# Performance work log

Hardware: AMD Instinct MI355X
Metric: run time of the kernel (lower is better)

The kernel has to match this reference:

```python
import jax
import jax.numpy as jnp
from jax import lax
import numpy as np

NUM_LABELS = 128
PAD, BOS, EOS = 0, 1, 2
B, T = 512, 512
NEG = -10000.0


def setup_inputs() -> dict:
    key = jax.random.key(0)
    k1, k2, k3, k4 = jax.random.split(key, 4)
    features = jax.random.normal(k1, (B, T, NUM_LABELS), dtype=jnp.float32)
    tag_seqs = jax.random.randint(k2, (B, T), 0, NUM_LABELS, dtype=jnp.int32)
    # prefix-valid mask with variable lengths in [T//2, T]
    lengths = jax.random.randint(k3, (B,), T // 2, T + 1, dtype=jnp.int32)
    mask = jnp.arange(T, dtype=jnp.int32)[None, :] < lengths[:, None]
    # transitions: randn then the constrained rows/cols from CRF.__init__
    tr = jax.random.normal(k4, (NUM_LABELS, NUM_LABELS), dtype=jnp.float32)
    tr = tr.at[:, BOS].set(NEG)
    tr = tr.at[EOS, :].set(NEG)
    tr = tr.at[PAD, :].set(NEG)
    tr = tr.at[:, PAD].set(NEG)
    tr = tr.at[PAD, PAD].set(0.0)
    tr = tr.at[PAD, EOS].set(0.0)
    return {"features": features, "tag_seqs": tag_seqs, "mask": mask, "transitions": tr}


def _crf_nll(features, transitions, tag_seqs, mask):
    maskf = mask.astype(features.dtype)  # [B,T]
    # ---- gold path score (score_sentences), fully vectorized over time ----
    emis = jnp.take_along_axis(features, tag_seqs[..., None], axis=-1)[..., 0]  # [B,T]
    trans_steps = transitions[tag_seqs[:, :-1], tag_seqs[:, 1:]]               # [B,T-1]
    gold = emis[:, 0] + transitions[BOS, tag_seqs[:, 0]]
    gold = gold + jnp.sum(maskf[:, 1:] * (emis[:, 1:] + trans_steps), axis=1)
    vlen = jnp.sum(mask.astype(jnp.int32), axis=1) - 1                          # [B]
    last_lab = jnp.take_along_axis(tag_seqs, vlen[:, None], axis=1)[:, 0]
    gold = gold + transitions[last_lab, EOS]
    # ---- log-partition (forward_alg): sequential scan over time ----
    init = transitions[BOS, :][None, :] + features[:, 0]  # [B,L]

    def step(fv, xs):
        feat_t, m_t = xs  # [B,L], [B] bool
        # scores[b, prev, cur] = fv[b,prev] + trans[prev,cur] + emit[b,cur]
        scores = fv[:, :, None] + transitions[None, :, :] + feat_t[:, None, :]
        new_fv = jax.nn.logsumexp(scores, axis=1)  # [B,L]
        fv = jnp.where(m_t[:, None], new_fv, fv)
        return fv, None

    xs = (jnp.swapaxes(features[:, 1:], 0, 1), jnp.swapaxes(mask[:, 1:], 0, 1))
    fv, _ = lax.scan(step, init, xs)
    logZ = jax.nn.logsumexp(fv + transitions[:, EOS][None, :], axis=-1)  # [B]
    return -jnp.mean(gold - logZ)


def reference(features, tag_seqs, mask, transitions):
    return _crf_nll(features, transitions, tag_seqs, mask)
```

## Files before the change

kernel.cpp:

```cpp
#include <hip/hip_runtime.h>
#include <cstdint>
#include <cstddef>

#define NLAB 128
#define TT   512
#define BB   512
#define MB   16
#define PAD_ 0
#define BOS_ 1
#define EOS_ 2
#define LN2F  0.6931471805599453f
#define LOG2E 1.4426950408889634f

typedef float f32x4 __attribute__((ext_vector_type(4)));
typedef short s16x8 __attribute__((ext_vector_type(8)));

#if __has_builtin(__builtin_amdgcn_exp2f)
#define EXP2F(x) __builtin_amdgcn_exp2f(x)
#else
#define EXP2F(x) exp2f(x)
#endif

#define MFMA_(A,B,CV) __builtin_amdgcn_mfma_f32_16x16x32_bf16((A),(B),(CV),0,0,0)

__device__ __forceinline__ bool mask_is_i32(const unsigned char* m8) {
    return m8[1] == 0;
}
__device__ __forceinline__ bool mask_at(const unsigned char* m8, int idx, bool isi) {
    if (isi) return ((const int*)m8)[idx] != 0;
    return m8[idx] != 0;
}

__device__ __forceinline__ unsigned f2bf(float f) {
    union { float f; unsigned u; } v; v.f = f;
    return (v.u + 0x7FFFu + ((v.u >> 16) & 1u)) >> 16;
}
__device__ __forceinline__ unsigned cvtpk(float lo, float hi) {
    unsigned r;
    asm("v_cvt_pk_bf16_f32 %0, %1, %2" : "=v"(r) : "v"(lo), "v"(hi));
    return r;
}

__global__ __launch_bounds__(256, 1) void crf_fused(
        const float* __restrict__ feats,
        const int*   __restrict__ tags,
        const unsigned char* __restrict__ m8,
        const float* __restrict__ tr,
        float* __restrict__ gold_out,
        float* __restrict__ logZ_out) {
    const int bx  = blockIdx.x;
    const int tid = threadIdx.x;
    const bool isi = mask_is_i32(m8);

    if (bx >= BB / MB) {
        const int b    = (bx - BB / MB) * 4 + (tid >> 6);
        const int lane = tid & 63;
        const size_t fb = (size_t)b * TT * NLAB;
        float gp = 0.f; int cnt = 0;
        for (int tt = lane; tt < TT; tt += 64) {
            const int idx = b * TT + tt;
            const bool mm = mask_at(m8, idx, isi);
            cnt += mm ? 1 : 0;
            const int tg = tags[idx];
            if (tt == 0) gp += feats[fb + tg] + tr[BOS_ * NLAB + tg];
            else if (mm) gp += feats[fb + (size_t)tt * NLAB + tg]
                             + tr[tags[idx - 1] * NLAB + tg];
        }
        #pragma unroll
        for (int off = 32; off > 0; off >>= 1) {
            gp  += __shfl_xor(gp,  off, 64);
            cnt += __shfl_xor(cnt, off, 64);
        }
        if (lane == 0)
            gold_out[b] = gp + tr[tags[b * TT + cnt - 1] * NLAB + EOS_];
        return;
    }

    const int w = tid >> 6;
    const int l = tid & 63;
    const int a = l >> 4;
    const int c = l & 15;
    const int G = bx * MB + c;
    const size_t fbase = (size_t)G * TT * NLAB;

    __shared__ __align__(16) unsigned short P16[2][2048];
    __shared__ float red_s[4][MB];

    f32x4 F0a, F0b, F1a, F1b, F2a, F2b, F3a, F3b,
          F4a, F4b, F5a, F5b, F6a, F6b, F7a, F7b;
    {
        const f32x4* fp = (const f32x4*)(feats + fbase);
        const int s0 = 4 * w + a, s1 = 4 * w + 16 + a;
        F0a = fp[1 * 32 + s0]; F0b = fp[1 * 32 + s1];
        F1a = fp[2 * 32 + s0]; F1b = fp[2 * 32 + s1];
        F2a = fp[3 * 32 + s0]; F2b = fp[3 * 32 + s1];
        F3a = fp[4 * 32 + s0]; F3b = fp[4 * 32 + s1];
        F4a = fp[5 * 32 + s0]; F4b = fp[5 * 32 + s1];
        F5a = fp[6 * 32 + s0]; F5b = fp[6 * 32 + s1];
        F6a = fp[7 * 32 + s0]; F6b = fp[7 * 32 + s1];
        F7a = fp[8 * 32 + s0]; F7b = fp[8 * 32 + s1];
    }

    int cnt = 0;
    if (isi) {
        const uint4* mp = (const uint4*)((const int*)m8 + (size_t)G * TT + a * 128);
        #pragma unroll 8
        for (int i = 0; i < 32; ++i) {
            uint4 v = mp[i];
            cnt += (v.x != 0) + (v.y != 0) + (v.z != 0) + (v.w != 0);
        }
    } else {
        const uint4* mp = (const uint4*)(m8 + (size_t)G * TT + a * 128);
        #pragma unroll
        for (int i = 0; i < 8; ++i) {
            uint4 v = mp[i];
            cnt += (int)((((v.x & 0x01010101u) * 0x01010101u) >> 24)
                       + (((v.y & 0x01010101u) * 0x01010101u) >> 24)
                       + (((v.z & 0x01010101u) * 0x01010101u) >> 24)
                       + (((v.w & 0x01010101u) * 0x01010101u) >> 24));
        }
    }
    cnt += __shfl_xor(cnt, 16, 64);
    cnt += __shfl_xor(cnt, 32, 64);
    const int mylen = cnt;
    int maxlen = mylen;
    maxlen = max(maxlen, __shfl_xor(maxlen, 1, 64));
    maxlen = max(maxlen, __shfl_xor(maxlen, 2, 64));
    maxlen = max(maxlen, __shfl_xor(maxlen, 4, 64));
    maxlen = max(maxlen, __shfl_xor(maxlen, 8, 64));
    const int mx = maxlen - 1;

    s16x8 Af00, Af01, Af02, Af03, Af10, Af11, Af12, Af13;
    {
        s16x8* A0[4] = {&Af00, &Af01, &Af02, &Af03};
        s16x8* A1[4] = {&Af10, &Af11, &Af12, &Af13};
        #pragma unroll
        for (int kt = 0; kt < 4; ++kt)
            #pragma unroll
            for (int jj = 0; jj < 8; ++jj) {
                const float* tp = tr + (kt * 32 + a * 8 + jj) * NLAB + c;
                (*A0[kt])[jj] = (short)f2bf(__expf(tp[w * 16]));
                (*A1[kt])[jj] = (short)f2bf(__expf(tp[(w + 4) * 16]));
            }
    }

    f32x4 pf0, pf1;
    float C;
    {
        const float n0 = tr[BOS_ * NLAB + 3] + feats[fbase + 3];
        C = n0;
        const f32x4 tb0 = *(const f32x4*)(tr + BOS_ * NLAB + w * 16 + a * 4);
        const f32x4 ff0 = *(const f32x4*)(feats + fbase + w * 16 + a * 4);
        const f32x4 tb1 = *(const f32x4*)(tr + BOS_ * NLAB + (w + 4) * 16 + a * 4);
        const f32x4 ff1 = *(const f32x4*)(feats + fbase + (w + 4) * 16 + a * 4);
        #pragma unroll
        for (int r = 0; r < 4; ++r) {
            pf0[r] = __expf(tb0[r] + ff0[r] - n0);
            pf1[r] = __expf(tb1[r] + ff1[r] - n0);
        }
    }

    const int wb0 = ((2 * w       + (a >> 1)) * 16 + c) * 8 + (a & 1) * 4;
    const int wb1 = ((2 * (w + 4) + (a >> 1)) * 16 + c) * 8 + (a & 1) * 4;
    *(uint2*)&P16[0][wb0] = make_uint2(cvtpk(pf0[0], pf0[1]), cvtpk(pf0[2], pf0[3]));
    *(uint2*)&P16[0][wb1] = make_uint2(cvtpk(pf1[0], pf1[1]), cvtpk(pf1[2], pf1[3]));

    const int rab = a * 16 + c;
    const f32x4 zac = {0.f, 0.f, 0.f, 0.f};

#define STEP(T_, Fa, Fb) {                                                    \
    __syncthreads();                                                          \
    const int PB = (T_) & 1;                                                  \
    const s16x8* PR = (const s16x8*)P16[1 - PB];                              \
    const s16x8 b0 = PR[rab],       b1 = PR[64 + rab],                        \
                b2 = PR[128 + rab], b3 = PR[192 + rab];                       \
    const int efield = ((int)(unsigned short)b0[3] >> 7) & 255;               \
    const int e = __shfl(efield, c, 64) - 126;                                \
    f32x4 x0 = MFMA_(Af00, b0, zac); x0 = MFMA_(Af01, b1, x0);                \
    f32x4 y0 = MFMA_(Af02, b2, zac); y0 = MFMA_(Af03, b3, y0);                \
    f32x4 x1 = MFMA_(Af10, b0, zac); x1 = MFMA_(Af11, b1, x1);                \
    f32x4 y1 = MFMA_(Af12, b2, zac); y1 = MFMA_(Af13, b3, y1);                \
    const float sc = __uint_as_float((unsigned)(127 - e) << 23);    \
    const f32x4 acc0 = x0 + y0, acc1 = x1 + y1;                               \
    const bool live = (T_) < mylen;                                           \
    _Pragma("unroll")                                                         \
    for (int r = 0; r < 4; ++r) {                                             \
        const float q0 = acc0[r] * (EXP2F(Fa[r] * LOG2E) * sc);               \
        const float q1 = acc1[r] * (EXP2F(Fb[r] * LOG2E) * sc);               \
        if (live) { pf0[r] = q0; pf1[r] = q1; }                               \
    }                                                                         \
    if (live) C += (float)e * LN2F;                                           \
    *(uint2*)&P16[PB][wb0] = make_uint2(cvtpk(pf0[0], pf0[1]),                \
                                        cvtpk(pf0[2], pf0[3]));               \
    *(uint2*)&P16[PB][wb1] = make_uint2(cvtpk(pf1[0], pf1[1]),                \
                                        cvtpk(pf1[2], pf1[3]));               \
}

    #pragma unroll 1
    for (int t0 = 1; t0 < maxlen; t0 += 8) {
        const int nstep = min(8, maxlen - t0);
        STEP(t0, F0a, F0b)
        if (nstep > 1) STEP(t0 + 1, F1a, F1b)
        if (nstep > 2) STEP(t0 + 2, F2a, F2b)
        if (nstep > 3) STEP(t0 + 3, F3a, F3b)
        if (nstep > 4) STEP(t0 + 4, F4a, F4b)
        if (nstep > 5) STEP(t0 + 5, F5a, F5b)
        if (nstep > 6) STEP(t0 + 6, F6a, F6b)
        if (nstep > 7) STEP(t0 + 7, F7a, F7b)
        if (t0 + 8 < maxlen) {
            const int s0 = 4 * w + a, s1 = 4 * w + 16 + a;
            const f32x4* fp;
#define RF(i, Xa, Xb)                                                         \
            fp = (const f32x4*)(feats + fbase                                 \
                     + (size_t)min(t0 + 8 + (i), mx) * NLAB);                 \
            Xa = fp[s0]; Xb = fp[s1];
            RF(0, F0a, F0b) RF(1, F1a, F1b) RF(2, F2a, F2b) RF(3, F3a, F3b)
            RF(4, F4a, F4b) RF(5, F5a, F5b) RF(6, F6a, F6b) RF(7, F7a, F7b)
#undef RF
        }
    }
#undef STEP

    float s = 0.f;
    #pragma unroll
    for (int r = 0; r < 4; ++r) {
        s += pf0[r] * __expf(tr[(w * 16 + 4 * a + r) * NLAB + EOS_]);
        s += pf1[r] * __expf(tr[((w + 4) * 16 + 4 * a + r) * NLAB + EOS_]);
    }
    s += __shfl_xor(s, 16, 64);
    s += __shfl_xor(s, 32, 64);
    if (l < 16) red_s[w][c] = s;
    __syncthreads();
    if (tid < 16) {
        float S = red_s[0][tid] + red_s[1][tid] + red_s[2][tid] + red_s[3][tid];
        logZ_out[bx * MB + tid] = C + __logf(S);
    }
}

__global__ void crf_finalize(const float* __restrict__ gold,
                             const float* __restrict__ logZ,
                             float* __restrict__ out) {
    __shared__ float sh[4];
    const int i = threadIdx.x;
    float v = (logZ[i] - gold[i]) + (logZ[i + 256] - gold[i + 256]);
    #pragma unroll
    for (int off = 32; off > 0; off >>= 1)
        v += __shfl_xor(v, off, 64);
    if ((i & 63) == 0) sh[i >> 6] = v;
    __syncthreads();
    if (i == 0) out[0] = (sh[0] + sh[1] + sh[2] + sh[3]) * (1.0f / (float)BB);
}

extern "C" void kernel_launch(void* const* d_in, const int* in_sizes, int n_in,
                              void* d_out, int out_size, void* d_ws, size_t ws_size,
                              hipStream_t stream) {
    const float*         feats = (const float*)d_in[0];
    const int*           tags  = (const int*)d_in[1];
    const unsigned char* m8    = (const unsigned char*)d_in[2];
    const float*         tr    = (const float*)d_in[3];

    float* gold = (float*)d_ws;
    float* logZ = gold + BB;
    float* out  = (float*)d_out;

    hipLaunchKernelGGL(crf_fused, dim3(BB / MB + BB / 4), dim3(256), 0, stream,
                       feats, tags, m8, tr, gold, logZ);
    hipLaunchKernelGGL(crf_finalize, dim3(1), dim3(256), 0, stream,
                       gold, logZ, out);
}
```

Measured before the change: 411.1 us.

## Stream feature prefetch per step and precompute next-step exponentials off critical path

Replaces the batched 8-step feature reload with a rolling per-step prefetch of the feature row eight steps ahead into the register that was just consumed. The emission exponential for the next step is computed after the LDS write, moving it off the critical path between barrier and MFMA result. The MFMA chain is split into eight independent products summed afterward, and the scale exponent is read straight from LDS instead of through a shuffle. This trades more frequent global loads and extra register pressure for shorter dependent latency inside each sequential scan step.

```diff
diff --git a/kernel.cpp b/kernel.cpp
--- a/kernel.cpp
+++ b/kernel.cpp
@@ -86,11 +86,12 @@
     __shared__ __align__(16) unsigned short P16[2][2048];
     __shared__ float red_s[4][MB];
 
+    const int s0 = 4 * w + a, s1 = 4 * w + 16 + a;
+
     f32x4 F0a, F0b, F1a, F1b, F2a, F2b, F3a, F3b,
           F4a, F4b, F5a, F5b, F6a, F6b, F7a, F7b;
     {
         const f32x4* fp = (const f32x4*)(feats + fbase);
-        const int s0 = 4 * w + a, s1 = 4 * w + 16 + a;
         F0a = fp[1 * 32 + s0]; F0b = fp[1 * 32 + s1];
         F1a = fp[2 * 32 + s0]; F1b = fp[2 * 32 + s1];
         F2a = fp[3 * 32 + s0]; F2b = fp[3 * 32 + s1];
@@ -165,28 +166,41 @@
     *(uint2*)&P16[0][wb0] = make_uint2(cvtpk(pf0[0], pf0[1]), cvtpk(pf0[2], pf0[3]));
     *(uint2*)&P16[0][wb1] = make_uint2(cvtpk(pf1[0], pf1[1]), cvtpk(pf1[2], pf1[3]));
 
+    #pragma unroll
+    for (int r = 0; r < 4; ++r) {
+        F0a[r] = EXP2F(F0a[r] * LOG2E);
+        F0b[r] = EXP2F(F0b[r] * LOG2E);
+    }
+
     const int rab = a * 16 + c;
     const f32x4 zac = {0.f, 0.f, 0.f, 0.f};
 
-#define STEP(T_, Fa, Fb) {                                                    \
+#define STEP(T_, Fa, Fb, Na, Nb) {                                            \
     __syncthreads();                                                          \
+    const f32x4 efa = Fa, efb = Fb;          \
+    {   const f32x4* fp = (const f32x4*)(feats + fbase                        \
+                              + (size_t)min((T_) + 8, mx) * NLAB);            \
+        Fa = fp[s0]; Fb = fp[s1]; }                                           \
     const int PB = (T_) & 1;                                                  \
     const s16x8* PR = (const s16x8*)P16[1 - PB];                              \
     const s16x8 b0 = PR[rab],       b1 = PR[64 + rab],                        \
                 b2 = PR[128 + rab], b3 = PR[192 + rab];                       \
-    const int efield = ((int)(unsigned short)b0[3] >> 7) & 255;               \
-    const int e = __shfl(efield, c, 64) - 126;                                \
-    f32x4 x0 = MFMA_(Af00, b0, zac); x0 = MFMA_(Af01, b1, x0);                \
-    f32x4 y0 = MFMA_(Af02, b2, zac); y0 = MFMA_(Af03, b3, y0);                \
-    f32x4 x1 = MFMA_(Af10, b0, zac); x1 = MFMA_(Af11, b1, x1);                \
-    f32x4 y1 = MFMA_(Af12, b2, zac); y1 = MFMA_(Af13, b3, y1);                \
+    const int p3 = (int)P16[1 - PB][c * 8 + 3];                               \
+    f32x4 x0 = MFMA_(Af00, b0, zac); f32x4 x1 = MFMA_(Af01, b1, zac);         \
+    f32x4 x2 = MFMA_(Af02, b2, zac); f32x4 x3 = MFMA_(Af03, b3, zac);         \
+    f32x4 y0 = MFMA_(Af10, b0, zac); f32x4 y1 = MFMA_(Af11, b1, zac);         \
+    f32x4 y2 = MFMA_(Af12, b2, zac); f32x4 y3 = MFMA_(Af13, b3, zac);         \
+    const int e = ((p3 >> 7) & 255) - 126;                                    \
     const float sc = __uint_as_float((unsigned)(127 - e) << 23);    \
-    const f32x4 acc0 = x0 + y0, acc1 = x1 + y1;                               \
+    const f32x4 acc0 = (x0 + x1) + (x2 + x3);                                 \
+    const f32x4 acc1 = (y0 + y1) + (y2 + y3);                                 \
     const bool live = (T_) < mylen;                                           \
     _Pragma("unroll")                                                         \
     for (int r = 0; r < 4; ++r) {                                             \
-        const float q0 = acc0[r] * (EXP2F(Fa[r] * LOG2E) * sc);               \
-        const float q1 = acc1[r] * (EXP2F(Fb[r] * LOG2E) * sc);               \
+        const float m0 = efa[r] * sc;      \
+        const float m1 = efb[r] * sc;                                         \
+        const float q0 = acc0[r] * m0;                                        \
+        const float q1 = acc1[r] * m1;                                        \
         if (live) { pf0[r] = q0; pf1[r] = q1; }                               \
     }                                                                         \
     if (live) C += (float)e * LN2F;                                           \
@@ -194,30 +208,24 @@
                                         cvtpk(pf0[2], pf0[3]));               \
     *(uint2*)&P16[PB][wb1] = make_uint2(cvtpk(pf1[0], pf1[1]),                \
                                         cvtpk(pf1[2], pf1[3]));               \
+    _Pragma("unroll")                                                         \
+    for (int r = 0; r < 4; ++r) {            \
+        Na[r] = EXP2F(Na[r] * LOG2E);                                         \
+        Nb[r] = EXP2F(Nb[r] * LOG2E);                                         \
+    }                                                                         \
 }
 
     #pragma unroll 1
     for (int t0 = 1; t0 < maxlen; t0 += 8) {
-        const int nstep = min(8, maxlen - t0);
-        STEP(t0, F0a, F0b)
-        if (nstep > 1) STEP(t0 + 1, F1a, F1b)
-        if (nstep > 2) STEP(t0 + 2, F2a, F2b)
-        if (nstep > 3) STEP(t0 + 3, F3a, F3b)
-        if (nstep > 4) STEP(t0 + 4, F4a, F4b)
-        if (nstep > 5) STEP(t0 + 5, F5a, F5b)
-        if (nstep > 6) STEP(t0 + 6, F6a, F6b)
-        if (nstep > 7) STEP(t0 + 7, F7a, F7b)
-        if (t0 + 8 < maxlen) {
-            const int s0 = 4 * w + a, s1 = 4 * w + 16 + a;
-            const f32x4* fp;
-#define RF(i, Xa, Xb)                                                         \
-            fp = (const f32x4*)(feats + fbase                                 \
-                     + (size_t)min(t0 + 8 + (i), mx) * NLAB);                 \
-            Xa = fp[s0]; Xb = fp[s1];
-            RF(0, F0a, F0b) RF(1, F1a, F1b) RF(2, F2a, F2b) RF(3, F3a, F3b)
-            RF(4, F4a, F4b) RF(5, F5a, F5b) RF(6, F6a, F6b) RF(7, F7a, F7b)
-#undef RF
-        }
+        const int nstep = maxlen - t0;
+        STEP(t0, F0a, F0b, F1a, F1b)
+        if (nstep > 1) STEP(t0 + 1, F1a, F1b, F2a, F2b)
+        if (nstep > 2) STEP(t0 + 2, F2a, F2b, F3a, F3b)
+        if (nstep > 3) STEP(t0 + 3, F3a, F3b, F4a, F4b)
+        if (nstep > 4) STEP(t0 + 4, F4a, F4b, F5a, F5b)
+        if (nstep > 5) STEP(t0 + 5, F5a, F5b, F6a, F6b)
+        if (nstep > 6) STEP(t0 + 6, F6a, F6b, F7a, F7b)
+        if (nstep > 7) STEP(t0 + 7, F7a, F7b, F0a, F0b)
     }
 #undef STEP
 
```

Measured after the change: 530.5 us. +29.1%, slower.
